# Kernel tuning notes

Hardware: AMD Instinct MI355X
Metric: run time of the kernel (lower is better)

Reference implementation:

```python
import jax, jax.numpy as jnp
import numpy as np

S_, H_, W_ = 7, 56, 56   # input_resolution
WS = 7                   # window_size
SHIFT = 3                # shift_size
GT = 1                   # gt_num (global tokens per window)
HEADS = 12
EPS = 1e-5


def _rel_pos_index(w):
    # replicates the torch buffer construction (incl. its 3*w-1 / 2*w-1 multipliers)
    coords = np.stack(np.meshgrid(np.arange(w), np.arange(w), np.arange(w), indexing='ij'))
    cf = coords.reshape(3, -1)
    rc = (cf[:, :, None] - cf[:, None, :]).transpose(1, 2, 0).astype(np.int64)
    rc += w - 1
    rc[..., 0] *= 3 * w - 1
    rc[..., 1] *= 2 * w - 1
    return rc.sum(-1)  # (w^3, w^3)


def _attn_mask(S, H, W, w, sh):
    # standard 3D shifted-window mask, built once from static shapes
    img = np.zeros((S, H, W))
    cnt = 0
    sls = (slice(0, -w), slice(-w, -sh), slice(-sh, None))
    for a in sls:
        for b in sls:
            for c in sls:
                img[a, b, c] = cnt
                cnt += 1
    m = img.reshape(S // w, w, H // w, w, W // w, w).transpose(0, 2, 4, 1, 3, 5).reshape(-1, w ** 3)
    d = m[:, None, :] - m[:, :, None]
    return np.where(d != 0, -100.0, 0.0).astype(np.float32)  # (nW, w^3, w^3)


def _ln(x, g, b):
    mu = jnp.mean(x, -1, keepdims=True)
    var = jnp.mean((x - mu) ** 2, -1, keepdims=True)
    return (x - mu) * jax.lax.rsqrt(var + EPS) * g + b


def setup_inputs() -> dict:
    key = jax.random.key(0)
    ks = jax.random.split(key, 7)
    C = 384
    hid = 4 * C
    L = S_ * H_ * W_
    nW = (S_ // WS) * (H_ // WS) * (W_ // WS)
    p = lambda k, shape: jax.random.normal(k, shape, jnp.float32) * 0.02
    return dict(
        x=jax.random.normal(ks[0], (1, L, C), jnp.float32),
        gt=jax.random.normal(ks[1], (nW, GT, C), jnp.float32),
        norm1_g=jnp.ones((C,), jnp.float32), norm1_b=jnp.zeros((C,), jnp.float32),
        qkv_w=p(ks[2], (C, 3 * C)), qkv_b=jnp.zeros((3 * C,), jnp.float32),
        bias_table=p(ks[3], ((2 * WS - 1) ** 3, HEADS)),
        proj_w=p(ks[4], (C, C)), proj_b=jnp.zeros((C,), jnp.float32),
        norm2_g=jnp.ones((C,), jnp.float32), norm2_b=jnp.zeros((C,), jnp.float32),
        fc1_w=p(ks[5], (C, hid)), fc1_b=jnp.zeros((hid,), jnp.float32),
        fc2_w=p(ks[6], (hid, C)), fc2_b=jnp.zeros((C,), jnp.float32),
    )


def _forward(x, gt, norm1_g, norm1_b, qkv_w, qkv_b, bias_table, proj_w, proj_b,
             norm2_g, norm2_b, fc1_w, fc1_b, fc2_w, fc2_b):
    B, L, C = x.shape
    h = HEADS
    d = C // h
    scale = d ** -0.5
    N_ = WS ** 3
    N = N_ + GT
    rpi = _rel_pos_index(WS)
    mask = jnp.asarray(_attn_mask(S_, H_, W_, WS, SHIFT))
    nW = mask.shape[0]

    shortcut = x
    xs = _ln(x, norm1_g, norm1_b).reshape(B, S_, H_, W_, C)
    xs = jnp.roll(xs, (-SHIFT, -SHIFT, -SHIFT), axis=(1, 2, 3))  # cyclic shift
    # window partition -> (B*nW, N_, C)
    xw = xs.reshape(B, S_ // WS, WS, H_ // WS, WS, W_ // WS, WS, C)
    xw = xw.transpose(0, 1, 3, 5, 2, 4, 6, 7).reshape(-1, N_, C)

    # --- WindowAttention with global tokens ---
    xc = jnp.concatenate([gt, xw], axis=1)  # (B*nW, N, C)
    qkv = (xc @ qkv_w + qkv_b).reshape(-1, N, 3, h, d).transpose(2, 0, 3, 1, 4)
    q, k, v = qkv[0] * scale, qkv[1], qkv[2]  # (B*nW, h, N, d)
    attn = jnp.einsum('bhnd,bhmd->bhnm', q, k)
    bias = bias_table[rpi.reshape(-1)].reshape(N_, N_, h).transpose(2, 0, 1)  # (h, N_, N_)
    bias = jnp.pad(bias, ((0, 0), (GT, 0), (GT, 0)))      # zeros on gt rows/cols == original submatrix add
    mpad = jnp.pad(mask, ((0, 0), (GT, 0), (GT, 0)))
    attn = attn + bias[None]
    attn = attn.reshape(B, nW, h, N, N) + mpad[None, :, None]
    attn = jax.nn.softmax(attn.reshape(-1, h, N, N), axis=-1)
    out = jnp.einsum('bhnm,bhmd->bhnd', attn, v).transpose(0, 2, 1, 3).reshape(-1, N, C)
    out = out @ proj_w + proj_b
    gt_out = out[:, :GT]
    xw = out[:, GT:]

    # window reverse + reverse shift
    xs = xw.reshape(B, S_ // WS, H_ // WS, W_ // WS, WS, WS, WS, C)
    xs = xs.transpose(0, 1, 4, 2, 5, 3, 6, 7).reshape(B, S_, H_, W_, C)
    xs = jnp.roll(xs, (SHIFT, SHIFT, SHIFT), axis=(1, 2, 3)).reshape(B, L, C)

    x = shortcut + xs  # drop_path = 0
    y = _ln(x, norm2_g, norm2_b)
    y = jax.nn.gelu(y @ fc1_w + fc1_b, approximate=False) @ fc2_w + fc2_b
    return x + y, gt_out


def reference(x, gt, norm1_g, norm1_b, qkv_w, qkv_b, bias_table, proj_w, proj_b,
              norm2_g, norm2_b, fc1_w, fc1_b, fc2_w, fc2_b):
    return _forward(x, gt, norm1_g, norm1_b, qkv_w, qkv_b, bias_table, proj_w, proj_b,
                    norm2_g, norm2_b, fc1_w, fc1_b, fc2_w, fc2_b)
```

## Files before the change

kernel.cpp:

```cpp
#include <hip/hip_runtime.h>
#include <math.h>

typedef __attribute__((ext_vector_type(8))) short short8;
typedef __attribute__((ext_vector_type(4))) float f32x4;
typedef __attribute__((ext_vector_type(4))) int i32x4;

__device__ __forceinline__ float b2f(short s) {
    unsigned u = ((unsigned)(unsigned short)s) << 16;
    return __builtin_bit_cast(float, u);
}
__device__ __forceinline__ short f2b(float f) {
    unsigned u = __builtin_bit_cast(unsigned, f);
    u += 0x7FFFu + ((u >> 16) & 1u);
    return (short)(u >> 16);
}
__device__ __forceinline__ int cvtpk(float lo, float hi) {
    int d;
    asm("v_cvt_pk_bf16_f32 %0, %1, %2" : "=v"(d) : "v"(lo), "v"(hi));
    return d;
}
__device__ __forceinline__ void gload16(const void* g, void* l) {
    __builtin_amdgcn_global_load_lds(
        (const __attribute__((address_space(1))) unsigned int*)g,
        (__attribute__((address_space(3))) unsigned int*)l, 16, 0, 0);
}

__global__ __launch_bounds__(256) void transpose_w(const float* __restrict__ src,
                                                   short* __restrict__ dst,
                                                   int K, int N) {
    __shared__ short tile[32][33];
    const int kt = blockIdx.y * 32, nt = blockIdx.x * 32;
    const int tx = threadIdx.x & 31, ty = threadIdx.x >> 5;
    #pragma unroll
    for (int i = 0; i < 4; i++) {
        int k = kt + ty + 8 * i, n = nt + tx;
        short v = 0;
        if (k < K && n < N) v = f2b(src[(size_t)k * N + n]);
        tile[ty + 8 * i][tx] = v;
    }
    __syncthreads();
    #pragma unroll
    for (int i = 0; i < 4; i++) {
        int n = nt + ty + 8 * i, k = kt + tx;
        if (n < N && k < K) dst[(size_t)n * K + k] = tile[tx][ty + 8 * i];
    }
}

__global__ void bias_pre(const float* __restrict__ btab, float* __restrict__ btf) {
    int idx = blockIdx.x * 256 + threadIdx.x;
    if (idx >= 4 * 12 * 22 * 11 * 2 * 64) return;
    int lane = idx & 63; int rem = idx >> 6;
    int h = rem & 1; rem >>= 1;
    int kk = rem % 11; rem /= 11;
    int rt = rem % 22; rem /= 22;
    int head = rem % 12; int cls = rem / 12;
    int i = rt * 16 + (lane & 15);
    int jbase = kk * 32 + (lane >> 4) * 8 + h * 4;
    f32x4 out;
    #pragma unroll
    for (int r = 0; r < 4; r++) {
        int jj = jbase + r;
        float v;
        if (jj >= 344) v = -1e30f;
        else if (i >= 344 || i == 0 || jj == 0) v = 0.f;
        else {
            int ti = i - 1, tj = jj - 1;
            int ai = ti / 49, bi = (ti % 49) / 7, ci = ti % 7;
            int aj = tj / 49, bj = (tj % 49) / 7, cj = tj % 7;
            int id3 = (ai - aj + 6) * 20 + (bi - bj + 6) * 13 + (ci - cj + 6);
            v = btab[id3 * 12 + head];
            int gsi = (ai < 4) ? 1 : 2, gsj = (aj < 4) ? 1 : 2;
            int ghi = (cls & 2) ? ((bi < 4) ? 1 : 2) : 0;
            int ghj = (cls & 2) ? ((bj < 4) ? 1 : 2) : 0;
            int gwi = (cls & 1) ? ((ci < 4) ? 1 : 2) : 0;
            int gwj = (cls & 1) ? ((cj < 4) ? 1 : 2) : 0;
            if (gsi != gsj || ghi != ghj || gwi != gwj) v -= 100.f;
        }
        out[r] = v;
    }
    *(f32x4*)&btf[(size_t)idx * 4] = out;
}

__global__ __launch_bounds__(256) void ln1_window(
    const float* __restrict__ x, const float* __restrict__ gt,
    const float* __restrict__ g, const float* __restrict__ b,
    short* __restrict__ xc)
{
    int wid = threadIdx.x >> 6, lane = threadIdx.x & 63;
    int r = blockIdx.x * 4 + wid;
    int w = r / 344, n = r - w * 344;
    if (n == 0) {
        #pragma unroll
        for (int i = 0; i < 6; i++) {
            int c = lane + i * 64;
            xc[(size_t)r * 384 + c] = f2b(gt[(size_t)w * 384 + c]);
        }
        return;
    }
    int t = n - 1;
    int a = t / 49, rm = t - a * 49, bb = rm / 7, cc = rm - bb * 7;
    int hw = w >> 3, ww = w & 7;
    int s = (a < 4) ? a + 3 : a - 4;
    int h = hw * 7 + bb + 3; if (h >= 56) h -= 56;
    int wd = ww * 7 + cc + 3; if (wd >= 56) wd -= 56;
    const float* row = x + (size_t)((s * 56 + h) * 56 + wd) * 384;
    float v[6]; float sum = 0.f;
    #pragma unroll
    for (int i = 0; i < 6; i++) { v[i] = row[lane + i * 64]; sum += v[i]; }
    #pragma unroll
    for (int off = 32; off >= 1; off >>= 1) sum += __shfl_xor(sum, off);
    float mu = sum * (1.0f / 384.0f);
    float vs = 0.f;
    #pragma unroll
    for (int i = 0; i < 6; i++) { float d = v[i] - mu; vs += d * d; }
    #pragma unroll
    for (int off = 32; off >= 1; off >>= 1) vs += __shfl_xor(vs, off);
    float rstd = rsqrtf(vs * (1.0f / 384.0f) + 1e-5f);
    #pragma unroll
    for (int i = 0; i < 6; i++) {
        int c = lane + i * 64;
        float o = (v[i] - mu) * rstd * g[c] + b[c];
        xc[(size_t)r * 384 + c] = f2b(o);
    }
}

__global__ __launch_bounds__(256) void ln2_kernel(
    const float* __restrict__ xn, const float* __restrict__ g,
    const float* __restrict__ b, short* __restrict__ out)
{
    int wid = threadIdx.x >> 6, lane = threadIdx.x & 63;
    int r = blockIdx.x * 4 + wid;
    const float* row = xn + (size_t)r * 384;
    float v[6]; float sum = 0.f;
    #pragma unroll
    for (int i = 0; i < 6; i++) { v[i] = row[lane + i * 64]; sum += v[i]; }
    #pragma unroll
    for (int off = 32; off >= 1; off >>= 1) sum += __shfl_xor(sum, off);
    float mu = sum * (1.0f / 384.0f);
    float vs = 0.f;
    #pragma unroll
    for (int i = 0; i < 6; i++) { float d = v[i] - mu; vs += d * d; }
    #pragma unroll
    for (int off = 32; off >= 1; off >>= 1) vs += __shfl_xor(vs, off);
    float rstd = rsqrtf(vs * (1.0f / 384.0f) + 1e-5f);
    #pragma unroll
    for (int i = 0; i < 6; i++) {
        int c = lane + i * 64;
        float o = (v[i] - mu) * rstd * g[c] + b[c];
        out[(size_t)r * 384 + c] = f2b(o);
    }
}

template<int EPI, bool QS>
__global__ __launch_bounds__(256, 4) void gemm128(
    const short* __restrict__ A, const short* __restrict__ BT,
    const float* __restrict__ bias, void* __restrict__ Out,
    const void* __restrict__ P0, void* __restrict__ P1,
    int M, int N, int K)
{
    __shared__ short As[128 * 64];
    __shared__ short Bs[128 * 64];
    const int m0 = blockIdx.y * 128, n0 = blockIdx.x * 128;
    const int tid = threadIdx.x;
    const int wid = tid >> 6, lane = tid & 63;
    const int wm = wid >> 1, wn = wid & 1;
    const int l15 = lane & 15, quad = lane >> 4;

    f32x4 acc[4][4];
    #pragma unroll
    for (int i = 0; i < 4; i++)
        #pragma unroll
        for (int j = 0; j < 4; j++) acc[i][j] = (f32x4){0.f, 0.f, 0.f, 0.f};

    const int trow = tid >> 3;
    const int cs = tid & 7;
    const int gc = cs ^ (trow & 7);
    const short* Ag[4]; const short* Bg[4];
    #pragma unroll
    for (int j = 0; j < 4; j++) {
        int ar = m0 + j * 32 + trow; if (ar >= M) ar = M - 1;
        Ag[j] = A + (size_t)ar * K + gc * 8;
        Bg[j] = BT + (size_t)(n0 + j * 32 + trow) * K + gc * 8;
    }
    short* AsW[4]; short* BsW[4];
    #pragma unroll
    for (int j = 0; j < 4; j++) {
        AsW[j] = &As[(j * 32 + wid * 8) * 64];
        BsW[j] = &Bs[(j * 32 + wid * 8) * 64];
    }
    int arow[4], brow[4];
    #pragma unroll
    for (int mt = 0; mt < 4; mt++) arow[mt] = wm * 64 + mt * 16 + l15;
    #pragma unroll
    for (int nt = 0; nt < 4; nt++) brow[nt] = wn * 64 + nt * 16 + l15;

    for (int ks = 0; ks < K; ks += 64) {
        #pragma unroll
        for (int j = 0; j < 4; j++) gload16(Ag[j] + ks, AsW[j]);
        #pragma unroll
        for (int j = 0; j < 4; j++) gload16(Bg[j] + ks, BsW[j]);
        __syncthreads();
        #pragma unroll
        for (int ko = 0; ko < 2; ko++) {
            short8 af[4], bf[4];
            #pragma unroll
            for (int mt = 0; mt < 4; mt++)
                af[mt] = *(const short8*)&As[arow[mt] * 64
                         + (((ko * 4 + quad) ^ (l15 & 7)) * 8)];
            #pragma unroll
            for (int nt = 0; nt < 4; nt++)
                bf[nt] = *(const short8*)&Bs[brow[nt] * 64
                         + (((ko * 4 + quad) ^ (l15 & 7)) * 8)];
            #pragma unroll
            for (int mt = 0; mt < 4; mt++)
                #pragma unroll
                for (int nt = 0; nt < 4; nt++)
                    acc[mt][nt] = __builtin_amdgcn_mfma_f32_16x16x32_bf16(
                        af[mt], bf[nt], acc[mt][nt], 0, 0, 0);
        }
        __syncthreads();
    }

    #pragma unroll
    for (int mt = 0; mt < 4; mt++) {
        #pragma unroll
        for (int nt = 0; nt < 4; nt++) {
            #pragma unroll
            for (int r = 0; r < 4; r++) {
                int row = m0 + wm * 64 + mt * 16 + quad * 4 + r;
                int col = n0 + wn * 64 + nt * 16 + l15;
                if (row >= M) continue;
                float v = acc[mt][nt][r] + bias[col];
                if (EPI == 0) {
                    if (QS && col < 384) v *= 0.17677669529663687f;
                    ((short*)Out)[(size_t)row * N + col] = f2b(v);
                } else if (EPI == 1) {
                    float u2 = v * v;
                    float w  = v * fmaf(0.07135481633f, u2, 1.5957691216f);
                    float e  = __expf(w);
                    float t  = __builtin_amdgcn_rcpf(1.0f + e);
                    v = v - v * t;
                    ((short*)Out)[(size_t)row * N + col] = f2b(v);
                } else if (EPI == 2) {
                    int w = row / 344, n = row - w * 344;
                    if (n == 0) {
                        ((float*)P1)[(size_t)w * 384 + col] = v;
                    } else {
                        int t = n - 1;
                        int a = t / 49, rm = t - a * 49;
                        int bb = rm / 7, cc = rm - bb * 7;
                        int hw = w >> 3, ww = w & 7;
                        int s = (a < 4) ? a + 3 : a - 4;
                        int h = hw * 7 + bb + 3; if (h >= 56) h -= 56;
                        int wd = ww * 7 + cc + 3; if (wd >= 56) wd -= 56;
                        size_t td = (size_t)((s * 56 + h) * 56 + wd) * 384 + col;
                        ((float*)Out)[td] = v + ((const float*)P0)[td];
                    }
                } else {
                    v += ((const float*)P0)[(size_t)row * N + col];
                    ((float*)Out)[(size_t)row * N + col] = v;
                }
            }
        }
    }
}

__global__ __launch_bounds__(256) void attn_kernel(
    const short* __restrict__ qkv, const float* __restrict__ btfm,
    short* __restrict__ attn_out)
{
    __shared__ short KT[352 * 32];
    __shared__ short VT[32 * 360];
    const int blk = blockIdx.x;
    const int w = blk / 12, head = blk - w * 12;
    const int cls = (((w >> 3) == 7) ? 2 : 0) | (((w & 7) == 7) ? 1 : 0);
    const int tid = threadIdx.x;
    const int wid = tid >> 6, lane = tid & 63;
    const int l15 = lane & 15, quad = lane >> 4;
    const size_t base = (size_t)w * 344 * 1152 + head * 32;

    for (int c = tid; c < 352 * 4; c += 256) {
        int n = c >> 2, ch = c & 3;
        short8 v8 = (short8){0,0,0,0,0,0,0,0};
        if (n < 344) v8 = *(const short8*)&qkv[base + 384 + (size_t)n * 1152 + ch * 8];
        int j32 = n & 31, kk = n >> 5;
        int R = kk * 32 + ((j32 >> 2) & 1) * 16 + ((j32 >> 3) << 2) + (j32 & 3);
        *(short8*)&KT[R * 32 + ((ch ^ ((R >> 1) & 3)) * 8)] = v8;
    }
    for (int e = tid; e < 344 * 4; e += 256) {
        int key = e >> 2, g = (e & 3) * 8;
        short8 v8 = *(const short8*)&qkv[base + 768 + (size_t)key * 1152 + g];
        #pragma unroll
        for (int i = 0; i < 8; i++) VT[(g + i) * 360 + key] = v8[i];
    }
    for (int e = tid; e < 8 * 32; e += 256) {
        int key = 344 + (e >> 5), dd = e & 31;
        VT[dd * 360 + key] = 0;
    }
    __syncthreads();

    const float* bh = btfm + (size_t)(cls * 12 + head) * (22 * 11 * 2 * 256);
    const int swq = (l15 >> 1) & 3;
    const int kOff = l15 * 32 + ((quad ^ swq) * 8);

    for (int j = wid; j < 11; j += 4) {
        const int rtA = 2 * j, rtB = rtA + 1;
        const int qrA = rtA * 16 + l15;
        int qrB = rtB * 16 + l15; if (qrB > 343) qrB = 343;
        short8 afA = *(const short8*)&qkv[base + (size_t)qrA * 1152 + quad * 8];
        short8 afB = *(const short8*)&qkv[base + (size_t)qrB * 1152 + quad * 8];

        f32x4 oA0 = {0,0,0,0}, oA1 = {0,0,0,0}, oB0 = {0,0,0,0}, oB1 = {0,0,0,0};
        float lA = 0.f, lB = 0.f;
        const float* bhA = bh + (size_t)rtA * (11 * 2 * 256) + lane * 4;
        const float* bhB = bh + (size_t)rtB * (11 * 2 * 256) + lane * 4;

        for (int kk = 0; kk < 11; kk++) {
            f32x4 cA0 = *(const f32x4*)&bhA[(kk * 2 + 0) * 256];
            f32x4 cA1 = *(const f32x4*)&bhA[(kk * 2 + 1) * 256];
            f32x4 cB0 = *(const f32x4*)&bhB[(kk * 2 + 0) * 256];
            f32x4 cB1 = *(const f32x4*)&bhB[(kk * 2 + 1) * 256];
            short8 k0 = *(const short8*)&KT[kk * 1024 + kOff];
            short8 k1 = *(const short8*)&KT[kk * 1024 + 512 + kOff];
            f32x4 sA0 = __builtin_amdgcn_mfma_f32_16x16x32_bf16(k0, afA, cA0, 0, 0, 0);
            f32x4 sA1 = __builtin_amdgcn_mfma_f32_16x16x32_bf16(k1, afA, cA1, 0, 0, 0);
            f32x4 sB0 = __builtin_amdgcn_mfma_f32_16x16x32_bf16(k0, afB, cB0, 0, 0, 0);
            f32x4 sB1 = __builtin_amdgcn_mfma_f32_16x16x32_bf16(k1, afB, cB1, 0, 0, 0);

            float a0 = __expf(sA0[0]), a1 = __expf(sA0[1]);
            float a2 = __expf(sA0[2]), a3 = __expf(sA0[3]);
            float a4 = __expf(sA1[0]), a5 = __expf(sA1[1]);
            float a6 = __expf(sA1[2]), a7 = __expf(sA1[3]);
            lA += ((a0 + a1) + (a2 + a3)) + ((a4 + a5) + (a6 + a7));
            i32x4 pkA;
            pkA[0] = cvtpk(a0, a1); pkA[1] = cvtpk(a2, a3);
            pkA[2] = cvtpk(a4, a5); pkA[3] = cvtpk(a6, a7);
            short8 paA = __builtin_bit_cast(short8, pkA);

            float b0 = __expf(sB0[0]), b1 = __expf(sB0[1]);
            float b2 = __expf(sB0[2]), b3 = __expf(sB0[3]);
            float b4 = __expf(sB1[0]), b5 = __expf(sB1[1]);
            float b6 = __expf(sB1[2]), b7 = __expf(sB1[3]);
            lB += ((b0 + b1) + (b2 + b3)) + ((b4 + b5) + (b6 + b7));
            i32x4 pkB;
            pkB[0] = cvtpk(b0, b1); pkB[1] = cvtpk(b2, b3);
            pkB[2] = cvtpk(b4, b5); pkB[3] = cvtpk(b6, b7);
            short8 paB = __builtin_bit_cast(short8, pkB);

            short8 v0 = *(const short8*)&VT[l15 * 360 + kk * 32 + quad * 8];
            short8 v1 = *(const short8*)&VT[(16 + l15) * 360 + kk * 32 + quad * 8];
            oA0 = __builtin_amdgcn_mfma_f32_16x16x32_bf16(paA, v0, oA0, 0, 0, 0);
            oA1 = __builtin_amdgcn_mfma_f32_16x16x32_bf16(paA, v1, oA1, 0, 0, 0);
            oB0 = __builtin_amdgcn_mfma_f32_16x16x32_bf16(paB, v0, oB0, 0, 0, 0);
            oB1 = __builtin_amdgcn_mfma_f32_16x16x32_bf16(paB, v1, oB1, 0, 0, 0);
        }

        lA += __shfl_xor(lA, 16); lA += __shfl_xor(lA, 32);
        lB += __shfl_xor(lB, 16); lB += __shfl_xor(lB, 32);
        float iA = 1.0f / lA, iB = 1.0f / lB;
        #pragma unroll
        for (int r = 0; r < 4; r++) {
            int rowA = rtA * 16 + quad * 4 + r;
            float nA = __shfl(iA, quad * 4 + r);
            float nB = __shfl(iB, quad * 4 + r);
            size_t obA = ((size_t)w * 344 + rowA) * 384 + head * 32;
            attn_out[obA + l15] = f2b(oA0[r] * nA);
            attn_out[obA + 16 + l15] = f2b(oA1[r] * nA);
            int rowB = rowA + 16;
            if (rowB < 344) {
                size_t obB = ((size_t)w * 344 + rowB) * 384 + head * 32;
                attn_out[obB + l15] = f2b(oB0[r] * nB);
                attn_out[obB + 16 + l15] = f2b(oB1[r] * nB);
            }
        }
    }
}

extern "C" void kernel_launch(void* const* d_in, const int* in_sizes, int n_in,
                              void* d_out, int out_size, void* d_ws, size_t ws_size,
                              hipStream_t stream)
{
    const float* x      = (const float*)d_in[0];
    const float* gt     = (const float*)d_in[1];
    const float* n1g    = (const float*)d_in[2];
    const float* n1b    = (const float*)d_in[3];
    const float* qkv_w  = (const float*)d_in[4];
    const float* qkv_b  = (const float*)d_in[5];
    const float* btab   = (const float*)d_in[6];
    const float* proj_w = (const float*)d_in[7];
    const float* proj_b = (const float*)d_in[8];
    const float* n2g    = (const float*)d_in[9];
    const float* n2b    = (const float*)d_in[10];
    const float* fc1_w  = (const float*)d_in[11];
    const float* fc1_b  = (const float*)d_in[12];
    const float* fc2_w  = (const float*)d_in[13];
    const float* fc2_b  = (const float*)d_in[14];

    char* ws = (char*)d_ws;
    short* wt_qkv  = (short*)(ws + 0);
    short* wt_proj = (short*)(ws + 884736);
    short* wt_fc1  = (short*)(ws + 1179648);
    short* wt_fc2  = (short*)(ws + 2359296);
    short* xc      = (short*)(ws + 3538944);
    short* qkvb    = (short*)(ws + 20447232);
    short* attn_o  = xc;
    short* h1      = (short*)(ws + 3538944);
    float* xnew    = (float*)(ws + 71172096);
    float* btfm    = (float*)(ws + 71172096);
    short* xnorm   = (short*)(ws + 104890368);

    float* outx  = (float*)d_out;
    float* outgt = outx + (size_t)21952 * 384;

    transpose_w<<<dim3(36, 12), 256, 0, stream>>>(qkv_w, wt_qkv, 384, 1152);
    transpose_w<<<dim3(12, 12), 256, 0, stream>>>(proj_w, wt_proj, 384, 384);
    transpose_w<<<dim3(48, 12), 256, 0, stream>>>(fc1_w, wt_fc1, 384, 1536);
    transpose_w<<<dim3(12, 48), 256, 0, stream>>>(fc2_w, wt_fc2, 1536, 384);

    bias_pre<<<dim3((4 * 12 * 22 * 11 * 2 * 64 + 255) / 256), 256, 0, stream>>>(btab, btfm);

    ln1_window<<<dim3(5504), 256, 0, stream>>>(x, gt, n1g, n1b, xc);

    gemm128<0, true><<<dim3(9, 172), 256, 0, stream>>>(xc, wt_qkv, qkv_b, qkvb,
                                                       nullptr, nullptr, 22016, 1152, 384);

    attn_kernel<<<dim3(768), 256, 0, stream>>>(qkvb, btfm, attn_o);

    gemm128<2, false><<<dim3(3, 172), 256, 0, stream>>>(attn_o, wt_proj, proj_b, xnew,
                                                        x, outgt, 22016, 384, 384);

    ln2_kernel<<<dim3(5488), 256, 0, stream>>>(xnew, n2g, n2b, xnorm);

    gemm128<1, false><<<dim3(12, 172), 256, 0, stream>>>(xnorm, wt_fc1, fc1_b, h1,
                                                         nullptr, nullptr, 21952, 1536, 384);

    gemm128<3, false><<<dim3(3, 172), 256, 0, stream>>>(h1, wt_fc2, fc2_b, outx,
                                                        xnew, nullptr, 21952, 384, 1536);
}
```

Before: 415.9 us.

## Fuse prep kernels, enlarge GEMM tile to 256x128, and remap attention blocks

```diff
diff --git a/kernel.cpp b/kernel.cpp
--- a/kernel.cpp
+++ b/kernel.cpp
@@ -25,11 +25,11 @@
         (__attribute__((address_space(3))) unsigned int*)l, 16, 0, 0);
 }
 
-__global__ __launch_bounds__(256) void transpose_w(const float* __restrict__ src,
-                                                   short* __restrict__ dst,
-                                                   int K, int N) {
-    __shared__ short tile[32][33];
-    const int kt = blockIdx.y * 32, nt = blockIdx.x * 32;
+__device__ __forceinline__ void transpose_body(
+    const float* __restrict__ src, short* __restrict__ dst,
+    int K, int N, int bx, int by, short (*tile)[33])
+{
+    const int kt = by * 32, nt = bx * 32;
     const int tx = threadIdx.x & 31, ty = threadIdx.x >> 5;
     #pragma unroll
     for (int i = 0; i < 4; i++) {
@@ -46,9 +46,10 @@
     }
 }
 
-__global__ void bias_pre(const float* __restrict__ btab, float* __restrict__ btf) {
-    int idx = blockIdx.x * 256 + threadIdx.x;
-    if (idx >= 4 * 12 * 22 * 11 * 2 * 64) return;
+__device__ __forceinline__ void bias_body(const float* __restrict__ btab,
+                                          float* __restrict__ btf, int blk)
+{
+    int idx = blk * 256 + threadIdx.x;
     int lane = idx & 63; int rem = idx >> 6;
     int h = rem & 1; rem >>= 1;
     int kk = rem % 11; rem /= 11;
@@ -81,13 +82,13 @@
     *(f32x4*)&btf[(size_t)idx * 4] = out;
 }
 
-__global__ __launch_bounds__(256) void ln1_window(
+__device__ __forceinline__ void ln1_body(
     const float* __restrict__ x, const float* __restrict__ gt,
     const float* __restrict__ g, const float* __restrict__ b,
-    short* __restrict__ xc)
+    short* __restrict__ xc, int blk)
 {
     int wid = threadIdx.x >> 6, lane = threadIdx.x & 63;
-    int r = blockIdx.x * 4 + wid;
+    int r = blk * 4 + wid;
     int w = r / 344, n = r - w * 344;
     if (n == 0) {
         #pragma unroll
@@ -124,6 +125,31 @@
     }
 }
 
+__global__ __launch_bounds__(256) void prep_kernel(
+    const float* __restrict__ qkv_w, const float* __restrict__ proj_w,
+    const float* __restrict__ fc1_w, const float* __restrict__ fc2_w,
+    short* __restrict__ wt_qkv, short* __restrict__ wt_proj,
+    short* __restrict__ wt_fc1, short* __restrict__ wt_fc2,
+    const float* __restrict__ btab, float* __restrict__ btf,
+    const float* __restrict__ x, const float* __restrict__ gt,
+    const float* __restrict__ n1g, const float* __restrict__ n1b,
+    short* __restrict__ xc)
+{
+    __shared__ short tile[32][33];
+    int b = blockIdx.x;
+    if (b < 432)  { transpose_body(qkv_w,  wt_qkv,  384, 1152, b % 36, b / 36, tile); return; }
+    b -= 432;
+    if (b < 144)  { transpose_body(proj_w, wt_proj, 384,  384, b % 12, b / 12, tile); return; }
+    b -= 144;
+    if (b < 576)  { transpose_body(fc1_w,  wt_fc1,  384, 1536, b % 48, b / 48, tile); return; }
+    b -= 576;
+    if (b < 576)  { transpose_body(fc2_w,  wt_fc2, 1536,  384, b % 12, b / 12, tile); return; }
+    b -= 576;
+    if (b < 5808) { bias_body(btab, btf, b); return; }
+    b -= 5808;
+    ln1_body(x, gt, n1g, n1b, xc, b);
+}
+
 __global__ __launch_bounds__(256) void ln2_kernel(
     const float* __restrict__ xn, const float* __restrict__ g,
     const float* __restrict__ b, short* __restrict__ out)
@@ -152,15 +178,15 @@
 }
 
 template<int EPI, bool QS>
-__global__ __launch_bounds__(256, 4) void gemm128(
+__global__ __launch_bounds__(512) void gemm256(
     const short* __restrict__ A, const short* __restrict__ BT,
     const float* __restrict__ bias, void* __restrict__ Out,
     const void* __restrict__ P0, void* __restrict__ P1,
     int M, int N, int K)
 {
-    __shared__ short As[128 * 64];
+    __shared__ short As[256 * 64];
     __shared__ short Bs[128 * 64];
-    const int m0 = blockIdx.y * 128, n0 = blockIdx.x * 128;
+    const int m0 = blockIdx.y * 256, n0 = blockIdx.x * 128;
     const int tid = threadIdx.x;
     const int wid = tid >> 6, lane = tid & 63;
     const int wm = wid >> 1, wn = wid & 1;
@@ -175,19 +201,23 @@
     const int trow = tid >> 3;
     const int cs = tid & 7;
     const int gc = cs ^ (trow & 7);
-    const short* Ag[4]; const short* Bg[4];
+    const short* Ag[4]; const short* Bg[2];
     #pragma unroll
     for (int j = 0; j < 4; j++) {
-        int ar = m0 + j * 32 + trow; if (ar >= M) ar = M - 1;
+        int ar = m0 + j * 64 + trow; if (ar >= M) ar = M - 1;
         Ag[j] = A + (size_t)ar * K + gc * 8;
-        Bg[j] = BT + (size_t)(n0 + j * 32 + trow) * K + gc * 8;
-    }
-    short* AsW[4]; short* BsW[4];
-    #pragma unroll
-    for (int j = 0; j < 4; j++) {
-        AsW[j] = &As[(j * 32 + wid * 8) * 64];
-        BsW[j] = &Bs[(j * 32 + wid * 8) * 64];
-    }
+    }
+    #pragma unroll
+    for (int j = 0; j < 2; j++) {
+        int br = n0 + j * 64 + trow; if (br >= N) br = N - 1;
+        Bg[j] = BT + (size_t)br * K + gc * 8;
+    }
+    short* AsW[4]; short* BsW[2];
+    #pragma unroll
+    for (int j = 0; j < 4; j++) AsW[j] = &As[(j * 64 + wid * 8) * 64];
+    #pragma unroll
+    for (int j = 0; j < 2; j++) BsW[j] = &Bs[(j * 64 + wid * 8) * 64];
+
     int arow[4], brow[4];
     #pragma unroll
     for (int mt = 0; mt < 4; mt++) arow[mt] = wm * 64 + mt * 16 + l15;
@@ -198,7 +228,7 @@
         #pragma unroll
         for (int j = 0; j < 4; j++) gload16(Ag[j] + ks, AsW[j]);
         #pragma unroll
-        for (int j = 0; j < 4; j++) gload16(Bg[j] + ks, BsW[j]);
+        for (int j = 0; j < 2; j++) gload16(Bg[j] + ks, BsW[j]);
         __syncthreads();
         #pragma unroll
         for (int ko = 0; ko < 2; ko++) {
@@ -271,8 +301,9 @@
 {
     __shared__ short KT[352 * 32];
     __shared__ short VT[32 * 360];
-    const int blk = blockIdx.x;
-    const int w = blk / 12, head = blk - w * 12;
+    const int orig = blockIdx.x;
+    const int nid = (orig & 7) * 96 + (orig >> 3);
+    const int head = nid >> 6, w = nid & 63;
     const int cls = (((w >> 3) == 7) ? 2 : 0) | (((w & 7) == 7) ? 1 : 0);
     const int tid = threadIdx.x;
     const int wid = tid >> 6, lane = tid & 63;
@@ -412,28 +443,23 @@
     float* outx  = (float*)d_out;
     float* outgt = outx + (size_t)21952 * 384;
 
-    transpose_w<<<dim3(36, 12), 256, 0, stream>>>(qkv_w, wt_qkv, 384, 1152);
-    transpose_w<<<dim3(12, 12), 256, 0, stream>>>(proj_w, wt_proj, 384, 384);
-    transpose_w<<<dim3(48, 12), 256, 0, stream>>>(fc1_w, wt_fc1, 384, 1536);
-    transpose_w<<<dim3(12, 48), 256, 0, stream>>>(fc2_w, wt_fc2, 1536, 384);
-
-    bias_pre<<<dim3((4 * 12 * 22 * 11 * 2 * 64 + 255) / 256), 256, 0, stream>>>(btab, btfm);
-
-    ln1_window<<<dim3(5504), 256, 0, stream>>>(x, gt, n1g, n1b, xc);
-
-    gemm128<0, true><<<dim3(9, 172), 256, 0, stream>>>(xc, wt_qkv, qkv_b, qkvb,
-                                                       nullptr, nullptr, 22016, 1152, 384);
+    prep_kernel<<<dim3(13040), 256, 0, stream>>>(
+        qkv_w, proj_w, fc1_w, fc2_w, wt_qkv, wt_proj, wt_fc1, wt_fc2,
+        btab, btfm, x, gt, n1g, n1b, xc);
+
+    gemm256<0, true><<<dim3(9, 86), 512, 0, stream>>>(xc, wt_qkv, qkv_b, qkvb,
+                                                      nullptr, nullptr, 22016, 1152, 384);
 
     attn_kernel<<<dim3(768), 256, 0, stream>>>(qkvb, btfm, attn_o);
 
-    gemm128<2, false><<<dim3(3, 172), 256, 0, stream>>>(attn_o, wt_proj, proj_b, xnew,
-                                                        x, outgt, 22016, 384, 384);
+    gemm256<2, false><<<dim3(3, 86), 512, 0, stream>>>(attn_o, wt_proj, proj_b, xnew,
+                                                       x, outgt, 22016, 384, 384);
 
     ln2_kernel<<<dim3(5488), 256, 0, stream>>>(xnew, n2g, n2b, xnorm);
 
-    gemm128<1, false><<<dim3(12, 172), 256, 0, stream>>>(xnorm, wt_fc1, fc1_b, h1,
-                                                         nullptr, nullptr, 21952, 1536, 384);
-
-    gemm128<3, false><<<dim3(3, 172), 256, 0, stream>>>(h1, wt_fc2, fc2_b, outx,
-                                                        xnew, nullptr, 21952, 384, 1536);
-}
+    gemm256<1, false><<<dim3(12, 86), 512, 0, stream>>>(xnorm, wt_fc1, fc1_b, h1,
+                                                        nullptr, nullptr, 21952, 1536, 384);
+
+    gemm256<3, false><<<dim3(3, 86), 512, 0, stream>>>(h1, wt_fc2, fc2_b, outx,
+                                                       xnew, nullptr, 21952, 384, 1536);
+}
```

Result: faster. 394.4 us (-5.2%).
